# Optimization experiments

Measured on AMD Instinct MI355X. Metric: run time of the kernel, lower is better.

The kernel has to match this reference:

```python
import jax, jax.numpy as jnp
import numpy as np

NUM_OBJ_CLS = 151  # Visual Genome object classes


def setup_inputs() -> dict:
    key = jax.random.key(0)
    ks = jax.random.split(key, 10)
    N_OBJ, HIDDEN, POOL, N_REL, N_RELCLS = 8192, 512, 4096, 32768, 51
    s = lambda d: 1.0 / np.sqrt(d)
    return {
        "edge_ctx": jax.random.normal(ks[0], (N_OBJ, HIDDEN), jnp.float32),
        "rel_pair_idx": jax.random.randint(ks[1], (N_REL, 2), 0, N_OBJ, jnp.int64),
        "union_features": jax.random.normal(ks[2], (N_REL, POOL), jnp.float32),
        "W_obj": jax.random.normal(ks[3], (HIDDEN, NUM_OBJ_CLS), jnp.float32) * s(HIDDEN),
        "b_obj": jnp.zeros((NUM_OBJ_CLS,), jnp.float32),
        "W_post_emb": jax.random.normal(ks[4], (HIDDEN, 2 * HIDDEN), jnp.float32) * s(HIDDEN),
        "b_post_emb": jnp.zeros((2 * HIDDEN,), jnp.float32),
        "W_post_cat": jax.random.normal(ks[5], (2 * HIDDEN, POOL), jnp.float32) * s(2 * HIDDEN),
        "b_post_cat": jnp.zeros((POOL,), jnp.float32),
        "W_rel": jax.random.normal(ks[6], (POOL, N_RELCLS), jnp.float32) * s(POOL),
        "b_rel": jnp.zeros((N_RELCLS,), jnp.float32),
        "freq_bias": jax.random.normal(ks[7], (NUM_OBJ_CLS * NUM_OBJ_CLS, N_RELCLS), jnp.float32),
    }


def reference(edge_ctx, rel_pair_idx, union_features, W_obj, b_obj,
              W_post_emb, b_post_emb, W_post_cat, b_post_cat, W_rel, b_rel,
              freq_bias):
    hidden = edge_ctx.shape[-1]
    # object classifier (stand-in for context layer's obj head)
    obj_dists = edge_ctx @ W_obj + b_obj                       # [N_obj, 151]
    obj_preds = jnp.argmax(obj_dists, axis=-1)                 # [N_obj]
    # post_emb -> split into head / tail representations
    edge_rep = (edge_ctx @ W_post_emb + b_post_emb).reshape(-1, 2, hidden)
    head_rep = edge_rep[:, 0]                                  # [N_obj, hidden]
    tail_rep = edge_rep[:, 1]
    # gather pair reps (global indices == per-image split + local gather + cat)
    h_idx, t_idx = rel_pair_idx[:, 0], rel_pair_idx[:, 1]
    prod_rep = jnp.concatenate([head_rep[h_idx], tail_rep[t_idx]], axis=-1)  # [N_rel, 2*hidden]
    prod_rep = prod_rep @ W_post_cat + b_post_cat              # [N_rel, pool]
    prod_rep = prod_rep * union_features                       # use_vision
    rel_dists = prod_rep @ W_rel + b_rel                       # [N_rel, 51]
    # frequency bias lookup on predicted (head, tail) label pairs
    pair_lbl = obj_preds[h_idx] * NUM_OBJ_CLS + obj_preds[t_idx]
    rel_dists = rel_dists + freq_bias[pair_lbl]
    return rel_dists
```

## Files before the change

### kernel.cpp

```cpp
#include <hip/hip_runtime.h>
#include <hip/hip_bf16.h>
#include <hip/hip_fp16.h>

typedef _Float16 f16;
typedef _Float16 f16x8 __attribute__((ext_vector_type(8)));
typedef _Float16 f16x4 __attribute__((ext_vector_type(4)));
typedef float f32x4 __attribute__((ext_vector_type(4)));

#define N_OBJ 8192
#define HIDDEN 512
#define POOL 4096
#define N_REL 32768
#define N_RELCLS 51
#define NUM_OBJ_CLS 151

#define WS_E16    0UL
#define WS_WPE16  8388608UL
#define WS_WCATT  9437184UL
#define WS_FT     17825792UL
#define WS_P      26214400UL
#define WS_BIAS   160432128UL
#define WS_PREDS  160448512UL
#define WS_WFRAG  160481280UL

typedef const __attribute__((address_space(1))) void* gas_ptr;
typedef __attribute__((address_space(3))) void* las_ptr;
__device__ __forceinline__ void gl_lds16(const f16* g, f16* l) {
    __builtin_amdgcn_global_load_lds((gas_ptr)g, (las_ptr)l, 16, 0, 0);
}

__global__ void k_convert(const float* __restrict__ in, f16* __restrict__ out, int n4) {
    int i = blockIdx.x * blockDim.x + threadIdx.x;
    if (i < n4) {
        f32x4 v = ((const f32x4*)in)[i];
        f16x4 h;
        h[0] = (f16)v[0]; h[1] = (f16)v[1]; h[2] = (f16)v[2]; h[3] = (f16)v[3];
        ((f16x4*)out)[i] = h;
    }
}

__global__ void k_transpose_cvt(const float* __restrict__ in, f16* __restrict__ out, int R, int C) {
    __shared__ float tile[32][33];
    int c0 = blockIdx.x * 32, r0 = blockIdx.y * 32;
    int tx = threadIdx.x, ty = threadIdx.y;
    #pragma unroll
    for (int i = 0; i < 4; i++)
        tile[ty + 8 * i][tx] = in[(size_t)(r0 + ty + 8 * i) * C + c0 + tx];
    __syncthreads();
    #pragma unroll
    for (int i = 0; i < 4; i++)
        out[(size_t)(c0 + ty + 8 * i) * R + r0 + tx] = (f16)tile[tx][ty + 8 * i];
}

__global__ __launch_bounds__(256) void k_bias(const float* __restrict__ b_pe, const float* __restrict__ Wcat,
                                              const float* __restrict__ b_cat, float* __restrict__ bias) {
    __shared__ float red[8][32];
    int c = blockIdx.x * 32 + (threadIdx.x & 31);
    int jq = threadIdx.x >> 5;
    float acc = 0.0f;
    #pragma unroll 4
    for (int j = jq * 128; j < jq * 128 + 128; j++)
        acc += b_pe[j] * Wcat[(size_t)j * POOL + c];
    red[jq][threadIdx.x & 31] = acc;
    __syncthreads();
    if (jq == 0) {
        float s = b_cat[c];
        #pragma unroll
        for (int q = 0; q < 8; q++) s += red[q][threadIdx.x & 31];
        bias[c] = s;
    }
}

#define OPB 8
__global__ __launch_bounds__(192) void k_argmax(const float* __restrict__ E, const float* __restrict__ Wobj,
                                                const float* __restrict__ bobj, int* __restrict__ preds) {
    __shared__ float se[OPB][HIDDEN];
    __shared__ double sv[OPB][NUM_OBJ_CLS];
    int o0 = blockIdx.x * OPB;
    for (int i = threadIdx.x; i < OPB * HIDDEN; i += 192)
        se[i / HIDDEN][i % HIDDEN] = E[(size_t)o0 * HIDDEN + i];
    __syncthreads();
    int j = threadIdx.x;
    if (j < NUM_OBJ_CLS) {
        double acc[OPB];
        double b = (double)bobj[j];
        #pragma unroll
        for (int o = 0; o < OPB; o++) acc[o] = b;
        for (int k = 0; k < HIDDEN; k++) {
            double w = (double)Wobj[(size_t)k * NUM_OBJ_CLS + j];
            #pragma unroll
            for (int o = 0; o < OPB; o++) acc[o] += (double)se[o][k] * w;
        }
        #pragma unroll
        for (int o = 0; o < OPB; o++) sv[o][j] = acc[o];
    }
    __syncthreads();
    if (threadIdx.x < OPB) {
        int o = threadIdx.x;
        double best = sv[o][0]; int bi = 0;
        for (int jj = 1; jj < NUM_OBJ_CLS; jj++) {
            double v = sv[o][jj];
            if (v > best) { best = v; bi = jj; }
        }
        preds[o0 + o] = bi;
    }
}

__global__ void k_wrel_frag(const float* __restrict__ Wrel, f16* __restrict__ frag) {
    int lane = threadIdx.x & 63;
    int nt = threadIdx.x >> 6;
    int kstep = blockIdx.x;
    int n = nt * 16 + (lane & 15);
    int k0 = kstep * 32 + (lane >> 4) * 8;
    f16x8 v;
    #pragma unroll
    for (int jj = 0; jj < 8; jj++) {
        float w = (n < N_RELCLS) ? Wrel[(size_t)(k0 + jj) * N_RELCLS + n] : 0.0f;
        v[jj] = (f16)w;
    }
    ((f16x8*)frag)[(size_t)(kstep * 4 + nt) * 64 + lane] = v;
}

template<bool SPLITM>
__global__ __launch_bounds__(256) void k_gemm(const f16* __restrict__ A, const f16* __restrict__ B,
                                              f16* __restrict__ C, const float* __restrict__ bias,
                                              int K, int lda, int ldb, int ldc,
                                              long aZ, long bZ, long cZ, int biasLimit) {
    __shared__ f16 As[128 * 64];
    __shared__ f16 Bs[128 * 64];
    long z = blockIdx.z;
    A += z * aZ; B += z * bZ; C += z * cZ;

    int tid = threadIdx.x;
    int w = tid >> 6, lane = tid & 63;
    int wm = w >> 1, wn = w & 1;
    int lr = lane & 15, lg = lane >> 4;
    int mBase = blockIdx.y * 128;
    int nBase = blockIdx.x * 128;

    const f16* aSrc[4]; const f16* bSrc[4];
    f16* aDst[4]; f16* bDst[4];
    #pragma unroll
    for (int p = 0; p < 4; p++) {
        int c = p * 256 + tid;
        int row = c >> 3, slot = c & 7;
        int scol = (slot ^ (row & 7)) * 8;
        aSrc[p] = A + (size_t)(mBase + row) * lda + scol;
        bSrc[p] = B + (size_t)(nBase + row) * ldb + scol;
        aDst[p] = As + p * 2048 + w * 512;
        bDst[p] = Bs + p * 2048 + w * 512;
    }

    int swz = (lr & 7) << 4;
    f32x4 acc[4][4] = {};

    for (int k0 = 0; k0 < K; k0 += 64) {
        if (k0) __syncthreads();
        #pragma unroll
        for (int p = 0; p < 4; p++) {
            gl_lds16(aSrc[p] + k0, aDst[p]);
            gl_lds16(bSrc[p] + k0, bDst[p]);
        }
        __syncthreads();
        #pragma unroll
        for (int kh = 0; kh < 2; kh++) {
            f16x8 av[4], bv[4];
            int koff = ((kh * 64 + lg * 16) ^ swz) >> 1;
            #pragma unroll
            for (int i = 0; i < 4; i++) {
                av[i] = *(const f16x8*)(As + (wm * 64 + i * 16 + lr) * 64 + koff);
                bv[i] = *(const f16x8*)(Bs + (wn * 64 + i * 16 + lr) * 64 + koff);
            }
            #pragma unroll
            for (int i = 0; i < 4; i++)
                #pragma unroll
                for (int jj = 0; jj < 4; jj++)
                    acc[i][jj] = __builtin_amdgcn_mfma_f32_16x16x32_f16(av[i], bv[jj], acc[i][jj], 0, 0, 0);
        }
    }

    #pragma unroll
    for (int i = 0; i < 4; i++) {
        int mb = mBase + wm * 64 + i * 16 + lg * 4;
        f32x4 bi = {};
        if (bias && mb < biasLimit) bi = *(const f32x4*)(bias + mb);
        #pragma unroll
        for (int jj = 0; jj < 4; jj++) {
            int n = nBase + wn * 64 + jj * 16 + lr;
            f16x4 hv;
            #pragma unroll
            for (int r = 0; r < 4; r++) hv[r] = (f16)(acc[i][jj][r] + bi[r]);
            if (SPLITM) {
                size_t off = ((size_t)((mb >= POOL) ? N_OBJ : 0) + n) * POOL + (mb & (POOL - 1));
                *(f16x4*)(C + off) = hv;
            } else {
                *(f16x4*)(C + (size_t)n * ldc + mb) = hv;
            }
        }
    }
}

__global__ __launch_bounds__(256) void k_final(const f16* __restrict__ P, const float* __restrict__ U,
                                               const int* __restrict__ relp, const int* __restrict__ preds,
                                               const f16* __restrict__ wfrag, const float* __restrict__ brel,
                                               const float* __restrict__ fbias, float* __restrict__ out) {
    int w = threadIdx.x >> 6;
    int lane = threadIdx.x & 63;
    int lr = lane & 15, lg = lane >> 4;
    int r0 = blockIdx.x * 64 + w * 16;
    int arow = r0 + lr;
    int h = relp[2 * arow], t = relp[2 * arow + 1];
    const f16* ph = P + (size_t)h * POOL;
    const f16* pt = P + (size_t)(N_OBJ + t) * POOL;
    const float* u = U + (size_t)arow * POOL;
    f32x4 acc[4] = {};
    for (int ks = 0; ks < POOL / 32; ks++) {
        int ka = ks * 32 + lg * 8;
        f16x8 vh = *(const f16x8*)(ph + ka);
        f16x8 vt = *(const f16x8*)(pt + ka);
        f32x4 u0 = __builtin_nontemporal_load((const f32x4*)(u + ka));
        f32x4 u1 = __builtin_nontemporal_load((const f32x4*)(u + ka + 4));
        f16x8 a;
        #pragma unroll
        for (int jj = 0; jj < 8; jj++) {
            float uu = (jj < 4) ? u0[jj] : u1[jj - 4];
            a[jj] = (f16)(((float)vh[jj] + (float)vt[jj]) * uu);
        }
        const f16x8* bf = (const f16x8*)wfrag + (size_t)ks * 4 * 64 + lane;
        #pragma unroll
        for (int nt = 0; nt < 4; nt++)
            acc[nt] = __builtin_amdgcn_mfma_f32_16x16x32_f16(a, bf[nt * 64], acc[nt], 0, 0, 0);
    }
    #pragma unroll
    for (int r = 0; r < 4; r++) {
        int row = r0 + lg * 4 + r;
        int h2 = relp[2 * row], t2 = relp[2 * row + 1];
        int lbl = preds[h2] * NUM_OBJ_CLS + preds[t2];
        const float* fb = fbias + (size_t)lbl * N_RELCLS;
        #pragma unroll
        for (int nt = 0; nt < 4; nt++) {
            int j = nt * 16 + lr;
            if (j < N_RELCLS)
                out[(size_t)row * N_RELCLS + j] = acc[nt][r] + brel[j] + fb[j];
        }
    }
}

extern "C" void kernel_launch(void* const* d_in, const int* in_sizes, int n_in,
                              void* d_out, int out_size, void* d_ws, size_t ws_size,
                              hipStream_t stream) {
    const float* edge_ctx = (const float*)d_in[0];
    const int*   relp     = (const int*)d_in[1];
    const float* U        = (const float*)d_in[2];
    const float* Wobj     = (const float*)d_in[3];
    const float* bobj     = (const float*)d_in[4];
    const float* Wpe      = (const float*)d_in[5];
    const float* bpe      = (const float*)d_in[6];
    const float* Wcat     = (const float*)d_in[7];
    const float* bcat     = (const float*)d_in[8];
    const float* Wrel     = (const float*)d_in[9];
    const float* brel     = (const float*)d_in[10];
    const float* fbias    = (const float*)d_in[11];
    float* out = (float*)d_out;

    char* ws = (char*)d_ws;
    f16*   E16    = (f16*)(ws + WS_E16);
    f16*   Wpe16  = (f16*)(ws + WS_WPE16);
    f16*   WcatT  = (f16*)(ws + WS_WCATT);
    f16*   FT     = (f16*)(ws + WS_FT);
    f16*   P      = (f16*)(ws + WS_P);
    float* bias   = (float*)(ws + WS_BIAS);
    int*   preds  = (int*)(ws + WS_PREDS);
    f16*   wfrag  = (f16*)(ws + WS_WFRAG);

    k_convert<<<4096, 256, 0, stream>>>(edge_ctx, E16, N_OBJ * HIDDEN / 4);
    k_convert<<<512, 256, 0, stream>>>(Wpe, Wpe16, HIDDEN * 2 * HIDDEN / 4);
    k_transpose_cvt<<<dim3(POOL / 32, (2 * HIDDEN) / 32), dim3(32, 8), 0, stream>>>(Wcat, WcatT, 2 * HIDDEN, POOL);
    k_bias<<<POOL / 32, 256, 0, stream>>>(bpe, Wcat, bcat, bias);
    k_argmax<<<N_OBJ / OPB, 192, 0, stream>>>(edge_ctx, Wobj, bobj, preds);
    k_wrel_frag<<<POOL / 32, 256, 0, stream>>>(Wrel, wfrag);
    k_gemm<false><<<dim3(POOL / 128, HIDDEN / 128, 2), 256, 0, stream>>>(
        Wpe16, WcatT, FT, nullptr, HIDDEN, 2 * HIDDEN, 2 * HIDDEN, HIDDEN,
        512L, 512L, (long)POOL * HIDDEN, 0);
    k_gemm<true><<<dim3(N_OBJ / 128, (2 * POOL) / 128, 1), 256, 0, stream>>>(
        FT, E16, P, bias, HIDDEN, HIDDEN, HIDDEN, POOL,
        0L, 0L, 0L, POOL);
    k_final<<<N_REL / 64, 256, 0, stream>>>(P, U, relp, preds, wfrag, brel, fbias, out);
}
```

Before: 405.8 us.

## Parallelize argmax over K-splits and split-K the final relation GEMM

The object-class argmax kernel drops its one-thread-per-class double loop. Instead, 256 threads each take a K-chunk and a strided class subset, use vectorized LDS reads, and combine partials with shuffles, LDS and a two-level argmax that breaks ties on the lowest index. The final fused gather/multiply/MFMA kernel now splits its K=4096 reduction between two wave pairs, combines them through LDS, and doubles the block count to 1024. This is meant to raise parallelism and memory-level concurrency in both kernels, at the cost of extra LDS traffic and barriers.

```diff
diff --git a/kernel.cpp b/kernel.cpp
--- a/kernel.cpp
+++ b/kernel.cpp
@@ -72,37 +72,106 @@
 }
 
 #define OPB 8
-__global__ __launch_bounds__(192) void k_argmax(const float* __restrict__ E, const float* __restrict__ Wobj,
+__global__ __launch_bounds__(256) void k_argmax(const float* __restrict__ E, const float* __restrict__ Wobj,
                                                 const float* __restrict__ bobj, int* __restrict__ preds) {
-    __shared__ float se[OPB][HIDDEN];
-    __shared__ double sv[OPB][NUM_OBJ_CLS];
+    __shared__ float se[OPB * HIDDEN];
+    __shared__ double part[2][OPB][5][32];
+    __shared__ double redv[OPB][32];
+    __shared__ int    redj[OPB][32];
+    int tid = threadIdx.x;
     int o0 = blockIdx.x * OPB;
-    for (int i = threadIdx.x; i < OPB * HIDDEN; i += 192)
-        se[i / HIDDEN][i % HIDDEN] = E[(size_t)o0 * HIDDEN + i];
-    __syncthreads();
-    int j = threadIdx.x;
-    if (j < NUM_OBJ_CLS) {
-        double acc[OPB];
-        double b = (double)bobj[j];
-        #pragma unroll
-        for (int o = 0; o < OPB; o++) acc[o] = b;
-        for (int k = 0; k < HIDDEN; k++) {
-            double w = (double)Wobj[(size_t)k * NUM_OBJ_CLS + j];
-            #pragma unroll
-            for (int o = 0; o < OPB; o++) acc[o] += (double)se[o][k] * w;
-        }
-        #pragma unroll
-        for (int o = 0; o < OPB; o++) sv[o][j] = acc[o];
-    }
-    __syncthreads();
-    if (threadIdx.x < OPB) {
-        int o = threadIdx.x;
-        double best = sv[o][0]; int bi = 0;
-        for (int jj = 1; jj < NUM_OBJ_CLS; jj++) {
-            double v = sv[o][jj];
-            if (v > best) { best = v; bi = jj; }
-        }
-        preds[o0 + o] = bi;
+    const f32x4* Ev = (const f32x4*)(E + (size_t)o0 * HIDDEN);
+    f32x4* sev = (f32x4*)se;
+    #pragma unroll
+    for (int i = 0; i < OPB * HIDDEN / 4 / 256; i++)
+        sev[tid + i * 256] = Ev[tid + i * 256];
+    __syncthreads();
+
+    int ks = tid >> 5;
+    int jg = tid & 31;
+    int jgc = (jg < 31) ? jg : 30;
+    double acc[OPB][5];
+    #pragma unroll
+    for (int o = 0; o < OPB; o++)
+        #pragma unroll
+        for (int jj = 0; jj < 5; jj++) acc[o][jj] = 0.0;
+
+    int kbase = ks * 64;
+    for (int k4 = 0; k4 < 16; k4++) {
+        int k = kbase + k4 * 4;
+        f32x4 ev[OPB];
+        #pragma unroll
+        for (int o = 0; o < OPB; o++) ev[o] = *(const f32x4*)(se + o * HIDDEN + k);
+        #pragma unroll
+        for (int kk = 0; kk < 4; kk++) {
+            const float* wrow = Wobj + (size_t)(k + kk) * NUM_OBJ_CLS;
+            float wv[5];
+            #pragma unroll
+            for (int jj = 0; jj < 5; jj++) {
+                int j = jj * 31 + jgc;
+                wv[jj] = wrow[(j < NUM_OBJ_CLS) ? j : (NUM_OBJ_CLS - 1)];
+            }
+            #pragma unroll
+            for (int o = 0; o < OPB; o++) {
+                double e = (double)ev[o][kk];
+                #pragma unroll
+                for (int jj = 0; jj < 5; jj++)
+                    acc[o][jj] = fma(e, (double)wv[jj], acc[o][jj]);
+            }
+        }
+    }
+
+    #pragma unroll
+    for (int o = 0; o < OPB; o++)
+        #pragma unroll
+        for (int jj = 0; jj < 5; jj++)
+            acc[o][jj] += __shfl_xor(acc[o][jj], 32);
+    int w = tid >> 6, lane = tid & 63;
+    if (w >= 2 && lane < 32) {
+        #pragma unroll
+        for (int o = 0; o < OPB; o++)
+            #pragma unroll
+            for (int jj = 0; jj < 5; jj++) part[w - 2][o][jj][lane] = acc[o][jj];
+    }
+    __syncthreads();
+    if (w < 2 && lane < 32) {
+        #pragma unroll
+        for (int o = 0; o < OPB; o++)
+            #pragma unroll
+            for (int jj = 0; jj < 5; jj++) acc[o][jj] += part[w][o][jj][lane];
+    }
+    __syncthreads();
+    if (w == 1 && lane < 32) {
+        #pragma unroll
+        for (int o = 0; o < OPB; o++)
+            #pragma unroll
+            for (int jj = 0; jj < 5; jj++) part[0][o][jj][lane] = acc[o][jj];
+    }
+    __syncthreads();
+    if (w == 0 && lane < 31) {
+        #pragma unroll
+        for (int o = 0; o < OPB; o++) {
+            double best = -1e300; int bj = NUM_OBJ_CLS;
+            #pragma unroll
+            for (int jj = 0; jj < 5; jj++) {
+                int j = jj * 31 + lane;
+                if (j < NUM_OBJ_CLS) {
+                    double v = acc[o][jj] + part[0][o][jj][lane] + (double)bobj[j];
+                    if (v > best || (v == best && j < bj)) { best = v; bj = j; }
+                }
+            }
+            redv[o][lane] = best; redj[o][lane] = bj;
+        }
+    }
+    __syncthreads();
+    if (tid < OPB) {
+        int o = tid;
+        double best = -1e300; int bj = NUM_OBJ_CLS;
+        for (int g = 0; g < 31; g++) {
+            double v = redv[o][g]; int j = redj[o][g];
+            if (v > best || (v == best && j < bj)) { best = v; bj = j; }
+        }
+        preds[o0 + o] = bj;
     }
 }
 
@@ -200,21 +269,25 @@
     }
 }
 
-__global__ __launch_bounds__(256) void k_final(const f16* __restrict__ P, const float* __restrict__ U,
-                                               const int* __restrict__ relp, const int* __restrict__ preds,
-                                               const f16* __restrict__ wfrag, const float* __restrict__ brel,
-                                               const float* __restrict__ fbias, float* __restrict__ out) {
+__global__ __launch_bounds__(256, 4) void k_final(const f16* __restrict__ P, const float* __restrict__ U,
+                                                  const int* __restrict__ relp, const int* __restrict__ preds,
+                                                  const f16* __restrict__ wfrag, const float* __restrict__ brel,
+                                                  const float* __restrict__ fbias, float* __restrict__ out) {
+    __shared__ f32x4 sacc[2][64][4];
     int w = threadIdx.x >> 6;
     int lane = threadIdx.x & 63;
+    int rg = w & 1, kh = w >> 1;
     int lr = lane & 15, lg = lane >> 4;
-    int r0 = blockIdx.x * 64 + w * 16;
+    int r0 = blockIdx.x * 32 + rg * 16;
     int arow = r0 + lr;
     int h = relp[2 * arow], t = relp[2 * arow + 1];
     const f16* ph = P + (size_t)h * POOL;
     const f16* pt = P + (size_t)(N_OBJ + t) * POOL;
     const float* u = U + (size_t)arow * POOL;
     f32x4 acc[4] = {};
-    for (int ks = 0; ks < POOL / 32; ks++) {
+    int ksEnd = kh * 64 + 64;
+    #pragma unroll 2
+    for (int ks = kh * 64; ks < ksEnd; ks++) {
         int ka = ks * 32 + lg * 8;
         f16x8 vh = *(const f16x8*)(ph + ka);
         f16x8 vt = *(const f16x8*)(pt + ka);
@@ -231,17 +304,26 @@
         for (int nt = 0; nt < 4; nt++)
             acc[nt] = __builtin_amdgcn_mfma_f32_16x16x32_f16(a, bf[nt * 64], acc[nt], 0, 0, 0);
     }
-    #pragma unroll
-    for (int r = 0; r < 4; r++) {
-        int row = r0 + lg * 4 + r;
-        int h2 = relp[2 * row], t2 = relp[2 * row + 1];
-        int lbl = preds[h2] * NUM_OBJ_CLS + preds[t2];
-        const float* fb = fbias + (size_t)lbl * N_RELCLS;
-        #pragma unroll
-        for (int nt = 0; nt < 4; nt++) {
-            int j = nt * 16 + lr;
-            if (j < N_RELCLS)
-                out[(size_t)row * N_RELCLS + j] = acc[nt][r] + brel[j] + fb[j];
+    if (kh == 1) {
+        #pragma unroll
+        for (int nt = 0; nt < 4; nt++) sacc[rg][lane][nt] = acc[nt];
+    }
+    __syncthreads();
+    if (kh == 0) {
+        #pragma unroll
+        for (int nt = 0; nt < 4; nt++) acc[nt] += sacc[rg][lane][nt];
+        #pragma unroll
+        for (int r = 0; r < 4; r++) {
+            int row = r0 + lg * 4 + r;
+            int h2 = relp[2 * row], t2 = relp[2 * row + 1];
+            int lbl = preds[h2] * NUM_OBJ_CLS + preds[t2];
+            const float* fb = fbias + (size_t)lbl * N_RELCLS;
+            #pragma unroll
+            for (int nt = 0; nt < 4; nt++) {
+                int j = nt * 16 + lr;
+                if (j < N_RELCLS)
+                    out[(size_t)row * N_RELCLS + j] = acc[nt][r] + brel[j] + fb[j];
+            }
         }
     }
 }
@@ -277,7 +359,7 @@
     k_convert<<<512, 256, 0, stream>>>(Wpe, Wpe16, HIDDEN * 2 * HIDDEN / 4);
     k_transpose_cvt<<<dim3(POOL / 32, (2 * HIDDEN) / 32), dim3(32, 8), 0, stream>>>(Wcat, WcatT, 2 * HIDDEN, POOL);
     k_bias<<<POOL / 32, 256, 0, stream>>>(bpe, Wcat, bcat, bias);
-    k_argmax<<<N_OBJ / OPB, 192, 0, stream>>>(edge_ctx, Wobj, bobj, preds);
+    k_argmax<<<N_OBJ / OPB, 256, 0, stream>>>(edge_ctx, Wobj, bobj, preds);
     k_wrel_frag<<<POOL / 32, 256, 0, stream>>>(Wrel, wfrag);
     k_gemm<false><<<dim3(POOL / 128, HIDDEN / 128, 2), 256, 0, stream>>>(
         Wpe16, WcatT, FT, nullptr, HIDDEN, 2 * HIDDEN, 2 * HIDDEN, HIDDEN,
@@ -285,5 +367,5 @@
     k_gemm<true><<<dim3(N_OBJ / 128, (2 * POOL) / 128, 1), 256, 0, stream>>>(
         FT, E16, P, bias, HIDDEN, HIDDEN, HIDDEN, POOL,
         0L, 0L, 0L, POOL);
-    k_final<<<N_REL / 64, 256, 0, stream>>>(P, U, relp, preds, wfrag, brel, fbias, out);
-}
+    k_final<<<N_REL / 32, 256, 0, stream>>>(P, U, relp, preds, wfrag, brel, fbias, out);
+}
```

Result: slower. 418.9 us (+3.2%).
